# Kernel tuning notes

Measured on AMD Instinct MI355X. Metric: run time of the kernel, lower is better.

The kernel has to match this reference:

```python
import jax, jax.numpy as jnp
import numpy as np

EPS = 1e-5

def layernorm(x, w, b):
    mu = jnp.mean(x, axis=-1, keepdims=True)
    xc = x - mu
    var = jnp.mean(xc * xc, axis=-1, keepdims=True)
    return xc * jax.lax.rsqrt(var + EPS) * w + b

def setup_inputs() -> dict:
    key = jax.random.key(0)
    ks = jax.random.split(key, 9)
    B, T, Nm, Nl = 8, 8, 1024, 64
    Vw, Tw, H, Dh = 1024, 2048, 8, 64
    inner = H * Dh  # 512
    s_q = 1.0 / np.sqrt(Tw)
    s_kv = 1.0 / np.sqrt(Vw)
    s_o = 1.0 / np.sqrt(inner)
    return {
        "x": jax.random.normal(ks[0], (B, T, Nm, Vw), jnp.float32),
        "latents": jax.random.normal(ks[1], (B, T, Nl, Tw), jnp.float32),
        "nm_w": jnp.ones((Vw,), jnp.float32),
        "nm_b": jnp.zeros((Vw,), jnp.float32),
        "nl_w": jnp.ones((Tw,), jnp.float32),
        "nl_b": jnp.zeros((Tw,), jnp.float32),
        "Wq": jax.random.normal(ks[2], (Tw, inner), jnp.float32) * s_q,
        "Wkv": jax.random.normal(ks[3], (Vw, 2 * inner), jnp.float32) * s_kv,
        "Wout": jax.random.normal(ks[4], (inner, Tw), jnp.float32) * s_o,
    }

def reference(x, latents, nm_w, nm_b, nl_w, nl_b, Wq, Wkv, Wout):
    H, Dh = 8, 64
    scale = Dh ** (-0.5)
    B, T, Nm, _ = x.shape
    Nl = latents.shape[2]
    xn = layernorm(x, nm_w, nm_b)          # (B,T,Nm,Vw)
    ln = layernorm(latents, nl_w, nl_b)    # (B,T,Nl,Tw)
    q = (ln @ Wq).reshape(B, T, Nl, H, Dh)           # b t i h d
    kv = xn @ Wkv                                     # (B,T,Nm,2*inner)
    k, v = jnp.split(kv, 2, axis=-1)
    k = k.reshape(B, T, Nm, H, Dh)                    # b t j h d
    v = v.reshape(B, T, Nm, H, Dh)
    sim = jnp.einsum('btihd,btjhd->bthij', q * scale, k)  # (B,T,H,Nl,Nm)
    attn = jax.nn.softmax(sim, axis=-1)
    out = jnp.einsum('bthij,btjhd->btihd', attn, v)       # (B,T,Nl,H,Dh)
    out = out.reshape(B, T, Nl, H * Dh)
    return out @ Wout                                     # (B,T,Nl,Tw)
```

## Files before the change

### kernel.cpp

```cpp
#include <hip/hip_runtime.h>

typedef __attribute__((ext_vector_type(8))) short bfrag8;
typedef __attribute__((ext_vector_type(4))) float f32x4;

typedef const unsigned int __attribute__((address_space(1)))* gas1_u32;
typedef unsigned int __attribute__((address_space(3)))* gas3_u32;

#define DEV __device__ __forceinline__

DEV unsigned short f2bf(float f) {
  unsigned int u = __builtin_bit_cast(unsigned int, f);
  u += 0x7fffu + ((u >> 16) & 1u);
  return (unsigned short)(u >> 16);
}

DEV void gload_lds16(const void* g, void* l) {
  __builtin_amdgcn_global_load_lds((gas1_u32)g, (gas3_u32)l, 16, 0, 0);
}

template<int N> DEV void gate_bar();
template<> DEV void gate_bar<4>() { asm volatile("s_waitcnt vmcnt(4)\n\ts_barrier" ::: "memory"); }
template<> DEV void gate_bar<6>() { asm volatile("s_waitcnt vmcnt(6)\n\ts_barrier" ::: "memory"); }
template<> DEV void gate_bar<8>() { asm volatile("s_waitcnt vmcnt(8)\n\ts_barrier" ::: "memory"); }

__global__ __launch_bounds__(256) void k_xstats(
    const float* __restrict__ x, unsigned short* __restrict__ xb,
    float* __restrict__ mu, float* __restrict__ rstd)
{
  const int wid = threadIdx.x >> 6, lane = threadIdx.x & 63;
  const int row = blockIdx.x * 4 + wid;
  const float* base = x + (size_t)row * 1024;
  float4 v[4];
  #pragma unroll
  for (int i = 0; i < 4; ++i) v[i] = ((const float4*)base)[i * 64 + lane];
  float s = 0.f, q = 0.f;
  #pragma unroll
  for (int i = 0; i < 4; ++i) {
    s += v[i].x + v[i].y + v[i].z + v[i].w;
    q += v[i].x*v[i].x + v[i].y*v[i].y + v[i].z*v[i].z + v[i].w*v[i].w;
  }
  #pragma unroll
  for (int off = 32; off >= 1; off >>= 1) { s += __shfl_xor(s, off); q += __shfl_xor(q, off); }
  const float m  = s * (1.0f/1024.0f);
  const float var = q * (1.0f/1024.0f) - m * m;
  const float rs = rsqrtf(var + 1e-5f);
  if (lane == 0) { mu[row] = m; rstd[row] = rs; }
  unsigned short* ob = xb + (size_t)row * 1024;
  #pragma unroll
  for (int i = 0; i < 4; ++i) {
    ushort4 o;
    o.x = f2bf(v[i].x); o.y = f2bf(v[i].y); o.z = f2bf(v[i].z); o.w = f2bf(v[i].w);
    ((ushort4*)ob)[i * 64 + lane] = o;
  }
}

__global__ __launch_bounds__(256) void k_lnlat(
    const float* __restrict__ lat, const float* __restrict__ w,
    const float* __restrict__ b, unsigned short* __restrict__ ln)
{
  const int row = blockIdx.x, tid = threadIdx.x;
  const float* base = lat + (size_t)row * 2048;
  const float4 v0 = ((const float4*)base)[tid];
  const float4 v1 = ((const float4*)base)[256 + tid];
  float s = v0.x+v0.y+v0.z+v0.w + v1.x+v1.y+v1.z+v1.w;
  float q = v0.x*v0.x+v0.y*v0.y+v0.z*v0.z+v0.w*v0.w
          + v1.x*v1.x+v1.y*v1.y+v1.z*v1.z+v1.w*v1.w;
  #pragma unroll
  for (int off = 32; off >= 1; off >>= 1) { s += __shfl_xor(s, off); q += __shfl_xor(q, off); }
  __shared__ float red[8];
  const int wid = tid >> 6, lane = tid & 63;
  if (lane == 0) { red[wid] = s; red[4 + wid] = q; }
  __syncthreads();
  s = red[0] + red[1] + red[2] + red[3];
  q = red[4] + red[5] + red[6] + red[7];
  const float m  = s * (1.0f/2048.0f);
  const float var = q * (1.0f/2048.0f) - m * m;
  const float rs = rsqrtf(var + 1e-5f);
  const float4 w0 = ((const float4*)w)[tid], w1 = ((const float4*)w)[256 + tid];
  const float4 b0 = ((const float4*)b)[tid], b1 = ((const float4*)b)[256 + tid];
  ushort4 o0, o1;
  o0.x = f2bf((v0.x - m) * rs * w0.x + b0.x);
  o0.y = f2bf((v0.y - m) * rs * w0.y + b0.y);
  o0.z = f2bf((v0.z - m) * rs * w0.z + b0.z);
  o0.w = f2bf((v0.w - m) * rs * w0.w + b0.w);
  o1.x = f2bf((v1.x - m) * rs * w1.x + b1.x);
  o1.y = f2bf((v1.y - m) * rs * w1.y + b1.y);
  o1.z = f2bf((v1.z - m) * rs * w1.z + b1.z);
  o1.w = f2bf((v1.w - m) * rs * w1.w + b1.w);
  ((ushort4*)(ln + (size_t)row * 2048))[tid] = o0;
  ((ushort4*)(ln + (size_t)row * 2048))[256 + tid] = o1;
}

__global__ __launch_bounds__(256) void k_transpose_cast(
    const float* __restrict__ src, unsigned short* __restrict__ dst,
    int K, int N, const float* __restrict__ rowscale, float scale)
{
  __shared__ float tile[32][33];
  const int tx = threadIdx.x & 31, ty = threadIdx.x >> 5;
  const int ntiles = N >> 5;
  const int k0 = (blockIdx.x / ntiles) << 5;
  const int n0 = (blockIdx.x % ntiles) << 5;
  #pragma unroll
  for (int r = 0; r < 4; ++r) {
    const int kk = ty + r * 8;
    float v = src[(size_t)(k0 + kk) * N + n0 + tx] * scale;
    if (rowscale) v *= rowscale[k0 + kk];
    tile[kk][tx] = v;
  }
  __syncthreads();
  #pragma unroll
  for (int r = 0; r < 4; ++r) {
    const int nn = ty + r * 8;
    dst[(size_t)(n0 + nn) * K + k0 + tx] = f2bf(tile[tx][nn]);
  }
}

__global__ __launch_bounds__(256) void k_c1c2_part(
    const float* __restrict__ Wkv, const float* __restrict__ w,
    const float* __restrict__ b, float* __restrict__ part)
{
  const int kc = blockIdx.x;
  const int n  = blockIdx.y * 256 + threadIdx.x;
  float s1 = 0.f, s2 = 0.f;
  const int k0 = kc * 64;
  for (int k = k0; k < k0 + 64; ++k) {
    const float wv = Wkv[(size_t)k * 1024 + n];
    s1 += w[k] * wv;
    s2 += b[k] * wv;
  }
  part[(size_t)(kc * 2 + 0) * 1024 + n] = s1;
  part[(size_t)(kc * 2 + 1) * 1024 + n] = s2;
}

__global__ __launch_bounds__(256) void k_c1c2_red(
    const float* __restrict__ part, float* __restrict__ c1, float* __restrict__ c2)
{
  const int n = blockIdx.x * 256 + threadIdx.x;
  float s1 = 0.f, s2 = 0.f;
  #pragma unroll
  for (int kc = 0; kc < 16; ++kc) {
    s1 += part[(size_t)(kc * 2 + 0) * 1024 + n];
    s2 += part[(size_t)(kc * 2 + 1) * 1024 + n];
  }
  c1[n] = s1; c2[n] = s2;
}

#define BAR8   __builtin_amdgcn_s_barrier()
#define GATE4  gate_bar<4>()

__global__ __launch_bounds__(512, 2) void k_gemm8(
    const unsigned short* __restrict__ A,
    const unsigned short* __restrict__ Bt,
    unsigned short* __restrict__ C,
    const float* __restrict__ mu, const float* __restrict__ rstd,
    const float* __restrict__ c1, const float* __restrict__ c2)
{
  constexpr int NKT = 16;
  __shared__ __attribute__((aligned(16))) char lds[131072];

  int bid = blockIdx.x;
  { const int nwg = gridDim.x; const int q = nwg >> 3; bid = (bid & 7) * q + (bid >> 3); }
  const int mt = bid >> 2, nt = bid & 3;
  const int tid = threadIdx.x;
  const int wid = tid >> 6, lane = tid & 63;
  const int g = lane >> 4, c = lane & 15;
  const int wr = wid >> 2, wc = wid & 3;
  const int MO = wr * 128, NO = wc * 64;

  const unsigned short* gA = A + (size_t)mt * 256 * 1024;
  const unsigned short* gB = Bt + (size_t)nt * 256 * 1024;

  const f32x4 zz = {0.f, 0.f, 0.f, 0.f};
  f32x4 acc[8][4];
  #pragma unroll
  for (int m = 0; m < 8; ++m)
    #pragma unroll
    for (int n = 0; n < 4; ++n) acc[m][n] = zz;

  auto stageA = [&](int buf, int kk, int kt) {
    #pragma unroll
    for (int i = 0; i < 2; ++i) {
      const int o = (i * 512 + tid) * 16;
      const int row = o >> 6;
      const int ss = ((((o >> 4) & 3) - (row >> 1)) & 3);
      gload_lds16((const char*)(gA + (size_t)row * 1024 + kt * 64 + kk * 32) + ss * 16,
                  lds + buf * 32768 + kk * 16384 + o);
    }
  };
  auto stageB = [&](int buf, int kk, int kt) {
    #pragma unroll
    for (int i = 0; i < 2; ++i) {
      const int o = (i * 512 + tid) * 16;
      const int row = o >> 6;
      const int ss = ((((o >> 4) & 3) - (row >> 1)) & 3);
      gload_lds16((const char*)(gB + (size_t)row * 1024 + kt * 64 + kk * 32) + ss * 16,
                  lds + 65536 + buf * 32768 + kk * 16384 + o);
    }
  };
  auto rdA = [&](int buf, int kk, int m) -> bfrag8 {
    const int row = MO + m * 16 + c;
    return *(const bfrag8*)(lds + buf * 32768 + kk * 16384 + row * 64
                            + (((g + (row >> 1)) & 3) << 4));
  };
  auto rdB = [&](int buf, int kk, int n) -> bfrag8 {
    const int row = NO + n * 16 + c;
    return *(const bfrag8*)(lds + 65536 + buf * 32768 + kk * 16384 + row * 64
                            + (((g + (row >> 1)) & 3) << 4));
  };

  bfrag8 a[8], b0[4], b1[4];

  auto tile4 = [&](int buf, int sb, int ukt) {
    #pragma unroll
    for (int m = 0; m < 8; ++m) a[m] = rdA(buf, 0, m);
    #pragma unroll
    for (int n = 0; n < 4; ++n) b0[n] = rdB(buf, 0, n);
    stageA(sb, 0, ukt);
    __builtin_amdgcn_s_setprio(1);
    #pragma unroll
    for (int m = 0; m < 8; ++m) {
      acc[m][0] = __builtin_amdgcn_mfma_f32_16x16x32_bf16(a[m], b0[0], acc[m][0], 0, 0, 0);
      acc[m][1] = __builtin_amdgcn_mfma_f32_16x16x32_bf16(a[m], b0[1], acc[m][1], 0, 0, 0);
    }
    __builtin_amdgcn_s_setprio(0);
    GATE4;
    #pragma unroll
    for (int n = 0; n < 4; ++n) b1[n] = rdB(buf, 1, n);
    stageB(sb, 0, ukt);
    __builtin_amdgcn_s_setprio(1);
    #pragma unroll
    for (int m = 0; m < 8; ++m) {
      acc[m][2] = __builtin_amdgcn_mfma_f32_16x16x32_bf16(a[m], b0[2], acc[m][2], 0, 0, 0);
      acc[m][3] = __builtin_amdgcn_mfma_f32_16x16x32_bf16(a[m], b0[3], acc[m][3], 0, 0, 0);
    }
    __builtin_amdgcn_s_setprio(0);
    GATE4;
    #pragma unroll
    for (int m = 0; m < 8; ++m) a[m] = rdA(buf, 1, m);
    stageB(sb, 1, ukt);
    __builtin_amdgcn_s_setprio(1);
    #pragma unroll
    for (int m = 0; m < 8; ++m) {
      acc[m][0] = __builtin_amdgcn_mfma_f32_16x16x32_bf16(a[m], b1[0], acc[m][0], 0, 0, 0);
      acc[m][1] = __builtin_amdgcn_mfma_f32_16x16x32_bf16(a[m], b1[1], acc[m][1], 0, 0, 0);
    }
    __builtin_amdgcn_s_setprio(0);
    BAR8;
    stageA(sb, 1, ukt);
    __builtin_amdgcn_s_setprio(1);
    #pragma unroll
    for (int m = 0; m < 8; ++m) {
      acc[m][2] = __builtin_amdgcn_mfma_f32_16x16x32_bf16(a[m], b1[2], acc[m][2], 0, 0, 0);
      acc[m][3] = __builtin_amdgcn_mfma_f32_16x16x32_bf16(a[m], b1[3], acc[m][3], 0, 0, 0);
    }
    __builtin_amdgcn_s_setprio(0);
    GATE4;
  };

  stageA(0, 0, 0); stageB(0, 0, 0); stageB(0, 1, 0); stageA(0, 1, 0);
  GATE4;

  for (int t = 0; t < NKT; t += 2) {
    const int u2 = (t + 2 < NKT) ? t + 2 : 0;
    tile4(0, 1, t + 1);
    tile4(1, 0, u2);
  }
  asm volatile("s_waitcnt vmcnt(0)" ::: "memory");

  #pragma unroll
  for (int m = 0; m < 8; ++m) {
    #pragma unroll
    for (int j = 0; j < 4; ++j) {
      const size_t orow = (size_t)mt * 256 + MO + m * 16 + g * 4 + j;
      const float rs = rstd[orow], muv = mu[orow];
      #pragma unroll
      for (int n = 0; n < 4; ++n) {
        const int gcol = nt * 256 + NO + n * 16 + c;
        const float v = rs * (acc[m][n][j] - muv * c1[gcol]) + c2[gcol];
        C[orow * 1024 + gcol] = f2bf(v);
      }
    }
  }
}

template<int BM, int BN, int WM, int WN, int NT, int MODE>
__global__ __launch_bounds__(NT, 2) void k_gemm(
    const unsigned short* __restrict__ A, int lda,
    const unsigned short* __restrict__ Bt, int ldb,
    int K, int mtiles, int ntiles,
    void* __restrict__ Cout, int ldc)
{
  constexpr int BK = 32;
  constexpr int NW = NT / 64;
  constexpr int MF = (BM / WM) / 16;
  constexpr int NF = (BN / WN) / 16;
  constexpr int LA = (BM * BK) / (8 * NT);
  constexpr int LB = (BN * BK) / (8 * NT);
  constexpr int LPS = LA + LB;
  constexpr int RA = BM * BK;
  constexpr int RB = BN * BK;
  static_assert(WM * WN == NW, "wave grid");
  static_assert(LA >= 1 && LB >= 1, "tile too small for NT");
  static_assert(LPS == 3 || LPS == 4, "gate specialization");

  __shared__ __attribute__((aligned(16))) unsigned short As[4 * RA];
  __shared__ __attribute__((aligned(16))) unsigned short Bs[4 * RB];

  int bid = blockIdx.x;
  {
    const int nwg = gridDim.x;
    if ((nwg & 7) == 0) {
      const int q = nwg >> 3;
      bid = (bid & 7) * q + (bid >> 3);
    }
  }
  const int mt = bid / ntiles, nt = bid % ntiles;
  const int tid = threadIdx.x;
  const int wid = tid >> 6, lane = tid & 63;
  const int g = lane >> 4, c = lane & 15;
  const int wr = wid / WN, wc = wid % WN;
  const int MO = wr * (BM / WM), NO = wc * (BN / WN);
  const int rot = (c >> 1) & 3;

  const unsigned short* gA = A + (size_t)mt * BM * lda;
  const unsigned short* gB = Bt + (size_t)nt * BN * ldb;

  const f32x4 zz = {0.f, 0.f, 0.f, 0.f};
  f32x4 acc[MF][NF];
  #pragma unroll
  for (int m = 0; m < MF; ++m)
    #pragma unroll
    for (int n = 0; n < NF; ++n) acc[m][n] = zz;

  auto stage = [&](int R, int kt) {
    #pragma unroll
    for (int i = 0; i < LA; ++i) {
      const int o = (i * NT + tid) * 16;
      const int row = o >> 6;
      const int slot = (o >> 4) & 3;
      const int srcb = (((slot - ((row >> 1) & 3)) & 3) << 4);
      gload_lds16((const char*)(gA + (size_t)row * lda + kt * BK) + srcb,
                  (char*)(As + R * RA) + o);
    }
    #pragma unroll
    for (int i = 0; i < LB; ++i) {
      const int o = (i * NT + tid) * 16;
      const int row = o >> 6;
      const int slot = (o >> 4) & 3;
      const int srcb = (((slot - ((row >> 1) & 3)) & 3) << 4);
      gload_lds16((const char*)(gB + (size_t)row * ldb + kt * BK) + srcb,
                  (char*)(Bs + R * RB) + o);
    }
  };

  auto compute = [&](int R) {
    const char* as = (const char*)(As + R * RA);
    const char* bs = (const char*)(Bs + R * RB);
    bfrag8 af[MF], bf[NF];
    #pragma unroll
    for (int m = 0; m < MF; ++m) {
      const int rw = MO + m * 16 + c;
      af[m] = *(const bfrag8*)(as + rw * 64 + (((g + rot) & 3) << 4));
    }
    #pragma unroll
    for (int n = 0; n < NF; ++n) {
      const int rw = NO + n * 16 + c;
      bf[n] = *(const bfrag8*)(bs + rw * 64 + (((g + rot) & 3) << 4));
    }
    #pragma unroll
    for (int m = 0; m < MF; ++m)
      #pragma unroll
      for (int n = 0; n < NF; ++n)
        acc[m][n] = __builtin_amdgcn_mfma_f32_16x16x32_bf16(af[m], bf[n], acc[m][n], 0, 0, 0);
  };

  const int nkt = K / BK;
  stage(0, 0); stage(1, 1); stage(2, 2);
  for (int t = 0; t < nkt; t += 4) {
    #pragma unroll
    for (int r = 0; r < 4; ++r) {
      int t3 = t + r + 3; if (t3 >= nkt) t3 -= nkt;
      gate_bar<2 * LPS>();
      stage((r + 3) & 3, t3);
      compute(r);
    }
  }
  asm volatile("s_waitcnt vmcnt(0)" ::: "memory");

  #pragma unroll
  for (int m = 0; m < MF; ++m) {
    #pragma unroll
    for (int j = 0; j < 4; ++j) {
      const size_t orow = (size_t)mt * BM + MO + m * 16 + g * 4 + j;
      #pragma unroll
      for (int n = 0; n < NF; ++n) {
        const int gcol = nt * BN + NO + n * 16 + c;
        const float v = acc[m][n][j];
        if constexpr (MODE == 2) ((float*)Cout)[orow * ldc + gcol] = v;
        else ((unsigned short*)Cout)[orow * ldc + gcol] = f2bf(v);
      }
    }
  }
}

__global__ __launch_bounds__(256) void k_attn(
    const unsigned short* __restrict__ q,
    const unsigned short* __restrict__ kv,
    unsigned short* __restrict__ ao)
{
  __shared__ __attribute__((aligned(16))) unsigned short Vt[64 * 64];
  const int bid = blockIdx.x;
  const int bt = bid >> 3, h = bid & 7;
  const int tid = threadIdx.x;
  const int wid = tid >> 6, lane = tid & 63;
  const int g = lane >> 4, c = lane & 15;

  const size_t qoff = ((size_t)bt * 64 + wid * 16 + c) * 512 + h * 64;
  const bfrag8 qf0 = *(const bfrag8*)(q + qoff + g * 8);
  const bfrag8 qf1 = *(const bfrag8*)(q + qoff + 32 + g * 8);

  const f32x4 zz = {0.f, 0.f, 0.f, 0.f};
  f32x4 o[4] = {zz, zz, zz, zz};
  float m_run = -1e30f, l_run = 0.f;

  const size_t kvbase = (size_t)bt * 1024 * 1024;
  const unsigned short* kbase = kv + kvbase + h * 64;
  const unsigned short* vbase = kv + kvbase + 512 + h * 64;

  for (int ch = 0; ch < 16; ++ch) {
    #pragma unroll
    for (int rr = 0; rr < 2; ++rr) {
      const int key = rr * 32 + (tid >> 3);
      const int d0 = (tid & 7) * 8;
      const bfrag8 vv = *(const bfrag8*)(vbase + (size_t)(ch * 64 + key) * 1024 + d0);
      #pragma unroll
      for (int j = 0; j < 8; ++j)
        Vt[(d0 + j) * 64 + (key ^ (j << 3))] = (unsigned short)vv[j];
    }
    __syncthreads();
    #pragma unroll
    for (int ks = 0; ks < 2; ++ks) {
      const int kb = ch * 64 + ks * 32;
      f32x4 s[2];
      #pragma unroll
      for (int t = 0; t < 2; ++t) {
        const int kr = ((c >> 2) << 3) + (t << 2) + (c & 3);
        const unsigned short* krow = kbase + (size_t)(kb + kr) * 1024;
        s[t] = zz;
        s[t] = __builtin_amdgcn_mfma_f32_16x16x32_bf16(*(const bfrag8*)(krow + g * 8),      qf0, s[t], 0, 0, 0);
        s[t] = __builtin_amdgcn_mfma_f32_16x16x32_bf16(*(const bfrag8*)(krow + 32 + g * 8), qf1, s[t], 0, 0, 0);
      }
      float pm = s[0][0];
      #pragma unroll
      for (int i = 1; i < 4; ++i) pm = fmaxf(pm, s[0][i]);
      #pragma unroll
      for (int i = 0; i < 4; ++i) pm = fmaxf(pm, s[1][i]);
      pm = fmaxf(pm, __shfl_xor(pm, 16));
      pm = fmaxf(pm, __shfl_xor(pm, 32));
      const float mn = fmaxf(m_run, pm);
      const float alpha = __expf(m_run - mn);
      float p[8];
      #pragma unroll
      for (int i = 0; i < 4; ++i) p[i]     = __expf(s[0][i] - mn);
      #pragma unroll
      for (int i = 0; i < 4; ++i) p[4 + i] = __expf(s[1][i] - mn);
      float ts = 0.f;
      #pragma unroll
      for (int i = 0; i < 8; ++i) ts += p[i];
      ts += __shfl_xor(ts, 16);
      ts += __shfl_xor(ts, 32);
      l_run = l_run * alpha + ts;
      m_run = mn;
      float ar[4];
      #pragma unroll
      for (int rj = 0; rj < 4; ++rj) ar[rj] = __shfl(alpha, g * 4 + rj);
      #pragma unroll
      for (int db = 0; db < 4; ++db)
        #pragma unroll
        for (int j = 0; j < 4; ++j) o[db][j] *= ar[j];
      bfrag8 pa;
      #pragma unroll
      for (int i = 0; i < 8; ++i) pa[i] = (short)f2bf(p[i]);
      #pragma unroll
      for (int db = 0; db < 4; ++db) {
        const int d = db * 16 + c;
        const bfrag8 vb = *(const bfrag8*)(Vt + d * 64 + ((ks * 32 + g * 8) ^ ((c & 7) << 3)));
        o[db] = __builtin_amdgcn_mfma_f32_16x16x32_bf16(pa, vb, o[db], 0, 0, 0);
      }
    }
    __syncthreads();
  }
  float lr[4];
  #pragma unroll
  for (int rj = 0; rj < 4; ++rj) lr[rj] = __shfl(l_run, g * 4 + rj);
  #pragma unroll
  for (int db = 0; db < 4; ++db)
    #pragma unroll
    for (int j = 0; j < 4; ++j) {
      const float val = o[db][j] / lr[j];
      ao[((size_t)bt * 64 + wid * 16 + g * 4 + j) * 512 + h * 64 + db * 16 + c] = f2bf(val);
    }
}

extern "C" void kernel_launch(void* const* d_in, const int* in_sizes, int n_in,
                              void* d_out, int out_size, void* d_ws, size_t ws_size,
                              hipStream_t stream)
{
  const float* x    = (const float*)d_in[0];
  const float* lat  = (const float*)d_in[1];
  const float* nm_w = (const float*)d_in[2];
  const float* nm_b = (const float*)d_in[3];
  const float* nl_w = (const float*)d_in[4];
  const float* nl_b = (const float*)d_in[5];
  const float* Wq   = (const float*)d_in[6];
  const float* Wkv  = (const float*)d_in[7];
  const float* Wout = (const float*)d_in[8];

  char* p = (char*)d_ws;
  auto take = [&](size_t bytes) { char* r = p; p += (bytes + 255) & ~(size_t)255; return r; };
  unsigned short* xb    = (unsigned short*)take(64ull * 1024 * 1024 * 2);
  unsigned short* kvb   = (unsigned short*)take(64ull * 1024 * 1024 * 2);
  unsigned short* lnb   = (unsigned short*)take(4096ull * 2048 * 2);
  unsigned short* qbuf  = (unsigned short*)take(4096ull * 512 * 2);
  unsigned short* aob   = (unsigned short*)take(4096ull * 512 * 2);
  unsigned short* WqT   = (unsigned short*)take(512ull * 2048 * 2);
  unsigned short* WkvT  = (unsigned short*)take(1024ull * 1024 * 2);
  unsigned short* WoutT = (unsigned short*)take(2048ull * 512 * 2);
  float* muv  = (float*)take(65536ull * 4);
  float* rsd  = (float*)take(65536ull * 4);
  float* c1   = (float*)take(1024 * 4);
  float* c2   = (float*)take(1024 * 4);
  float* part = (float*)take(32ull * 1024 * 4);
  if ((size_t)(p - (char*)d_ws) > ws_size) return;

  k_transpose_cast<<<dim3(64 * 16), 256, 0, stream>>>(Wq,   WqT,   2048,  512, nullptr, 0.125f);
  k_transpose_cast<<<dim3(32 * 32), 256, 0, stream>>>(Wkv,  WkvT,  1024, 1024, nm_w,    1.0f);
  k_transpose_cast<<<dim3(16 * 64), 256, 0, stream>>>(Wout, WoutT,  512, 2048, nullptr, 1.0f);
  k_c1c2_part<<<dim3(16, 4), 256, 0, stream>>>(Wkv, nm_w, nm_b, part);
  k_c1c2_red<<<dim3(4), 256, 0, stream>>>(part, c1, c2);
  k_xstats<<<dim3(16384), 256, 0, stream>>>(x, xb, muv, rsd);
  k_lnlat<<<dim3(4096), 256, 0, stream>>>(lat, nl_w, nl_b, lnb);

  k_gemm8<<<dim3(1024), 512, 0, stream>>>(xb, WkvT, kvb, muv, rsd, c1, c2);
  k_gemm<64, 128, 1, 4, 256, 1><<<dim3(256), 256, 0, stream>>>(
      lnb, 2048, WqT, 2048, 2048, 64, 4, qbuf, 512);

  k_attn<<<dim3(512), 256, 0, stream>>>(qbuf, kvb, aob);

  k_gemm<64, 128, 1, 4, 256, 2><<<dim3(1024), 256, 0, stream>>>(
      aob, 512, WoutT, 512, 512, 64, 16, d_out, 2048);
}
```

Baseline: 378.3 us.

## Write K/V/Q in head-major layout and fold latent layernorm into Q GEMM epilogue

The KV and Q GEMM epilogues now write outputs in a head-major (bt,h,j,d) layout, so attention reads K and V rows with a 64-element stride instead of 1024, giving contiguous per-head tiles. The latent layernorm is replaced by the shared stats kernel (raw bf16 cast plus mu/rstd), with nl_w folded into WqT and the mean/bias corrections applied through c1q/c2q in the Q GEMM epilogue. This removes the separate normalize pass and improves attention locality, at the cost of scattered epilogue stores and bf16 rounding of un-normalized latents.

```diff
diff --git a/kernel.cpp b/kernel.cpp
--- a/kernel.cpp
+++ b/kernel.cpp
@@ -23,72 +23,37 @@
 template<> DEV void gate_bar<6>() { asm volatile("s_waitcnt vmcnt(6)\n\ts_barrier" ::: "memory"); }
 template<> DEV void gate_bar<8>() { asm volatile("s_waitcnt vmcnt(8)\n\ts_barrier" ::: "memory"); }
 
-__global__ __launch_bounds__(256) void k_xstats(
+template<int W>
+__global__ __launch_bounds__(256) void k_stats(
     const float* __restrict__ x, unsigned short* __restrict__ xb,
     float* __restrict__ mu, float* __restrict__ rstd)
 {
+  constexpr int NV = W / 256;
   const int wid = threadIdx.x >> 6, lane = threadIdx.x & 63;
   const int row = blockIdx.x * 4 + wid;
-  const float* base = x + (size_t)row * 1024;
-  float4 v[4];
-  #pragma unroll
-  for (int i = 0; i < 4; ++i) v[i] = ((const float4*)base)[i * 64 + lane];
+  const float* base = x + (size_t)row * W;
+  float4 v[NV];
+  #pragma unroll
+  for (int i = 0; i < NV; ++i) v[i] = ((const float4*)base)[i * 64 + lane];
   float s = 0.f, q = 0.f;
   #pragma unroll
-  for (int i = 0; i < 4; ++i) {
+  for (int i = 0; i < NV; ++i) {
     s += v[i].x + v[i].y + v[i].z + v[i].w;
     q += v[i].x*v[i].x + v[i].y*v[i].y + v[i].z*v[i].z + v[i].w*v[i].w;
   }
   #pragma unroll
   for (int off = 32; off >= 1; off >>= 1) { s += __shfl_xor(s, off); q += __shfl_xor(q, off); }
-  const float m  = s * (1.0f/1024.0f);
-  const float var = q * (1.0f/1024.0f) - m * m;
-  const float rs = rsqrtf(var + 1e-5f);
+  const float m   = s * (1.0f / W);
+  const float var = q * (1.0f / W) - m * m;
+  const float rs  = rsqrtf(var + 1e-5f);
   if (lane == 0) { mu[row] = m; rstd[row] = rs; }
-  unsigned short* ob = xb + (size_t)row * 1024;
-  #pragma unroll
-  for (int i = 0; i < 4; ++i) {
+  unsigned short* ob = xb + (size_t)row * W;
+  #pragma unroll
+  for (int i = 0; i < NV; ++i) {
     ushort4 o;
     o.x = f2bf(v[i].x); o.y = f2bf(v[i].y); o.z = f2bf(v[i].z); o.w = f2bf(v[i].w);
     ((ushort4*)ob)[i * 64 + lane] = o;
   }
-}
-
-__global__ __launch_bounds__(256) void k_lnlat(
-    const float* __restrict__ lat, const float* __restrict__ w,
-    const float* __restrict__ b, unsigned short* __restrict__ ln)
-{
-  const int row = blockIdx.x, tid = threadIdx.x;
-  const float* base = lat + (size_t)row * 2048;
-  const float4 v0 = ((const float4*)base)[tid];
-  const float4 v1 = ((const float4*)base)[256 + tid];
-  float s = v0.x+v0.y+v0.z+v0.w + v1.x+v1.y+v1.z+v1.w;
-  float q = v0.x*v0.x+v0.y*v0.y+v0.z*v0.z+v0.w*v0.w
-          + v1.x*v1.x+v1.y*v1.y+v1.z*v1.z+v1.w*v1.w;
-  #pragma unroll
-  for (int off = 32; off >= 1; off >>= 1) { s += __shfl_xor(s, off); q += __shfl_xor(q, off); }
-  __shared__ float red[8];
-  const int wid = tid >> 6, lane = tid & 63;
-  if (lane == 0) { red[wid] = s; red[4 + wid] = q; }
-  __syncthreads();
-  s = red[0] + red[1] + red[2] + red[3];
-  q = red[4] + red[5] + red[6] + red[7];
-  const float m  = s * (1.0f/2048.0f);
-  const float var = q * (1.0f/2048.0f) - m * m;
-  const float rs = rsqrtf(var + 1e-5f);
-  const float4 w0 = ((const float4*)w)[tid], w1 = ((const float4*)w)[256 + tid];
-  const float4 b0 = ((const float4*)b)[tid], b1 = ((const float4*)b)[256 + tid];
-  ushort4 o0, o1;
-  o0.x = f2bf((v0.x - m) * rs * w0.x + b0.x);
-  o0.y = f2bf((v0.y - m) * rs * w0.y + b0.y);
-  o0.z = f2bf((v0.z - m) * rs * w0.z + b0.z);
-  o0.w = f2bf((v0.w - m) * rs * w0.w + b0.w);
-  o1.x = f2bf((v1.x - m) * rs * w1.x + b1.x);
-  o1.y = f2bf((v1.y - m) * rs * w1.y + b1.y);
-  o1.z = f2bf((v1.z - m) * rs * w1.z + b1.z);
-  o1.w = f2bf((v1.w - m) * rs * w1.w + b1.w);
-  ((ushort4*)(ln + (size_t)row * 2048))[tid] = o0;
-  ((ushort4*)(ln + (size_t)row * 2048))[256 + tid] = o1;
 }
 
 __global__ __launch_bounds__(256) void k_transpose_cast(
@@ -116,31 +81,31 @@
 }
 
 __global__ __launch_bounds__(256) void k_c1c2_part(
-    const float* __restrict__ Wkv, const float* __restrict__ w,
-    const float* __restrict__ b, float* __restrict__ part)
+    const float* __restrict__ Wm, const float* __restrict__ w,
+    const float* __restrict__ b, float* __restrict__ part, int N, float scale)
 {
   const int kc = blockIdx.x;
   const int n  = blockIdx.y * 256 + threadIdx.x;
   float s1 = 0.f, s2 = 0.f;
   const int k0 = kc * 64;
   for (int k = k0; k < k0 + 64; ++k) {
-    const float wv = Wkv[(size_t)k * 1024 + n];
+    const float wv = Wm[(size_t)k * N + n];
     s1 += w[k] * wv;
     s2 += b[k] * wv;
   }
-  part[(size_t)(kc * 2 + 0) * 1024 + n] = s1;
-  part[(size_t)(kc * 2 + 1) * 1024 + n] = s2;
+  part[(size_t)(kc * 2 + 0) * N + n] = s1 * scale;
+  part[(size_t)(kc * 2 + 1) * N + n] = s2 * scale;
 }
 
 __global__ __launch_bounds__(256) void k_c1c2_red(
-    const float* __restrict__ part, float* __restrict__ c1, float* __restrict__ c2)
+    const float* __restrict__ part, float* __restrict__ c1, float* __restrict__ c2,
+    int nchunks, int N)
 {
   const int n = blockIdx.x * 256 + threadIdx.x;
   float s1 = 0.f, s2 = 0.f;
-  #pragma unroll
-  for (int kc = 0; kc < 16; ++kc) {
-    s1 += part[(size_t)(kc * 2 + 0) * 1024 + n];
-    s2 += part[(size_t)(kc * 2 + 1) * 1024 + n];
+  for (int kc = 0; kc < nchunks; ++kc) {
+    s1 += part[(size_t)(kc * 2 + 0) * N + n];
+    s2 += part[(size_t)(kc * 2 + 1) * N + n];
   }
   c1[n] = s1; c2[n] = s2;
 }
@@ -151,7 +116,7 @@
 __global__ __launch_bounds__(512, 2) void k_gemm8(
     const unsigned short* __restrict__ A,
     const unsigned short* __restrict__ Bt,
-    unsigned short* __restrict__ C,
+    unsigned short* __restrict__ Chm,
     const float* __restrict__ mu, const float* __restrict__ rstd,
     const float* __restrict__ c1, const float* __restrict__ c2)
 {
@@ -272,12 +237,14 @@
     #pragma unroll
     for (int j = 0; j < 4; ++j) {
       const size_t orow = (size_t)mt * 256 + MO + m * 16 + g * 4 + j;
+      const int btn = (int)(orow >> 10), jj = (int)(orow & 1023);
+      const size_t pbase = ((size_t)(btn * 16 + nt * 4 + wc)) * 65536 + (size_t)jj * 64;
       const float rs = rstd[orow], muv = mu[orow];
       #pragma unroll
       for (int n = 0; n < 4; ++n) {
         const int gcol = nt * 256 + NO + n * 16 + c;
         const float v = rs * (acc[m][n][j] - muv * c1[gcol]) + c2[gcol];
-        C[orow * 1024 + gcol] = f2bf(v);
+        Chm[pbase + n * 16 + c] = f2bf(v);
       }
     }
   }
@@ -288,7 +255,9 @@
     const unsigned short* __restrict__ A, int lda,
     const unsigned short* __restrict__ Bt, int ldb,
     int K, int mtiles, int ntiles,
-    void* __restrict__ Cout, int ldc)
+    void* __restrict__ Cout, int ldc,
+    const float* __restrict__ mu, const float* __restrict__ rstd,
+    const float* __restrict__ c1, const float* __restrict__ c2)
 {
   constexpr int BK = 32;
   constexpr int NW = NT / 64;
@@ -392,20 +361,28 @@
     #pragma unroll
     for (int j = 0; j < 4; ++j) {
       const size_t orow = (size_t)mt * BM + MO + m * 16 + g * 4 + j;
+      float rs = 0.f, muv = 0.f;
+      if constexpr (MODE == 1) { rs = rstd[orow]; muv = mu[orow]; }
       #pragma unroll
       for (int n = 0; n < NF; ++n) {
         const int gcol = nt * BN + NO + n * 16 + c;
-        const float v = acc[m][n][j];
-        if constexpr (MODE == 2) ((float*)Cout)[orow * ldc + gcol] = v;
-        else ((unsigned short*)Cout)[orow * ldc + gcol] = f2bf(v);
+        float v = acc[m][n][j];
+        if constexpr (MODE == 1) {
+          v = rs * (v - muv * c1[gcol]) + c2[gcol];
+          const int bt = (int)(orow >> 6), ii = (int)(orow & 63);
+          const int h = gcol >> 6, d = gcol & 63;
+          ((unsigned short*)Cout)[(size_t)(bt * 8 + h) * 4096 + ii * 64 + d] = f2bf(v);
+        } else {
+          ((float*)Cout)[orow * ldc + gcol] = v;
+        }
       }
     }
   }
 }
 
 __global__ __launch_bounds__(256) void k_attn(
-    const unsigned short* __restrict__ q,
-    const unsigned short* __restrict__ kv,
+    const unsigned short* __restrict__ q2,
+    const unsigned short* __restrict__ kv2,
     unsigned short* __restrict__ ao)
 {
   __shared__ __attribute__((aligned(16))) unsigned short Vt[64 * 64];
@@ -415,24 +392,23 @@
   const int wid = tid >> 6, lane = tid & 63;
   const int g = lane >> 4, c = lane & 15;
 
-  const size_t qoff = ((size_t)bt * 64 + wid * 16 + c) * 512 + h * 64;
-  const bfrag8 qf0 = *(const bfrag8*)(q + qoff + g * 8);
-  const bfrag8 qf1 = *(const bfrag8*)(q + qoff + 32 + g * 8);
+  const size_t qoff = ((size_t)(bt * 8 + h) * 64 + wid * 16 + c) * 64;
+  const bfrag8 qf0 = *(const bfrag8*)(q2 + qoff + g * 8);
+  const bfrag8 qf1 = *(const bfrag8*)(q2 + qoff + 32 + g * 8);
 
   const f32x4 zz = {0.f, 0.f, 0.f, 0.f};
   f32x4 o[4] = {zz, zz, zz, zz};
   float m_run = -1e30f, l_run = 0.f;
 
-  const size_t kvbase = (size_t)bt * 1024 * 1024;
-  const unsigned short* kbase = kv + kvbase + h * 64;
-  const unsigned short* vbase = kv + kvbase + 512 + h * 64;
+  const unsigned short* kbase = kv2 + (size_t)(bt * 16 + h) * 65536;
+  const unsigned short* vbase = kv2 + (size_t)(bt * 16 + 8 + h) * 65536;
 
   for (int ch = 0; ch < 16; ++ch) {
     #pragma unroll
     for (int rr = 0; rr < 2; ++rr) {
       const int key = rr * 32 + (tid >> 3);
       const int d0 = (tid & 7) * 8;
-      const bfrag8 vv = *(const bfrag8*)(vbase + (size_t)(ch * 64 + key) * 1024 + d0);
+      const bfrag8 vv = *(const bfrag8*)(vbase + (size_t)(ch * 64 + key) * 64 + d0);
       #pragma unroll
       for (int j = 0; j < 8; ++j)
         Vt[(d0 + j) * 64 + (key ^ (j << 3))] = (unsigned short)vv[j];
@@ -445,7 +421,7 @@
       #pragma unroll
       for (int t = 0; t < 2; ++t) {
         const int kr = ((c >> 2) << 3) + (t << 2) + (c & 3);
-        const unsigned short* krow = kbase + (size_t)(kb + kr) * 1024;
+        const unsigned short* krow = kbase + (size_t)(kb + kr) * 64;
         s[t] = zz;
         s[t] = __builtin_amdgcn_mfma_f32_16x16x32_bf16(*(const bfrag8*)(krow + g * 8),      qf0, s[t], 0, 0, 0);
         s[t] = __builtin_amdgcn_mfma_f32_16x16x32_bf16(*(const bfrag8*)(krow + 32 + g * 8), qf1, s[t], 0, 0, 0);
@@ -520,7 +496,7 @@
   auto take = [&](size_t bytes) { char* r = p; p += (bytes + 255) & ~(size_t)255; return r; };
   unsigned short* xb    = (unsigned short*)take(64ull * 1024 * 1024 * 2);
   unsigned short* kvb   = (unsigned short*)take(64ull * 1024 * 1024 * 2);
-  unsigned short* lnb   = (unsigned short*)take(4096ull * 2048 * 2);
+  unsigned short* latb  = (unsigned short*)take(4096ull * 2048 * 2);
   unsigned short* qbuf  = (unsigned short*)take(4096ull * 512 * 2);
   unsigned short* aob   = (unsigned short*)take(4096ull * 512 * 2);
   unsigned short* WqT   = (unsigned short*)take(512ull * 2048 * 2);
@@ -528,25 +504,33 @@
   unsigned short* WoutT = (unsigned short*)take(2048ull * 512 * 2);
   float* muv  = (float*)take(65536ull * 4);
   float* rsd  = (float*)take(65536ull * 4);
+  float* mul  = (float*)take(4096ull * 4);
+  float* rsl  = (float*)take(4096ull * 4);
   float* c1   = (float*)take(1024 * 4);
   float* c2   = (float*)take(1024 * 4);
-  float* part = (float*)take(32ull * 1024 * 4);
+  float* c1q  = (float*)take(512 * 4);
+  float* c2q  = (float*)take(512 * 4);
+  float* part  = (float*)take(32ull * 1024 * 4);
+  float* part2 = (float*)take(64ull * 512 * 4);
   if ((size_t)(p - (char*)d_ws) > ws_size) return;
 
-  k_transpose_cast<<<dim3(64 * 16), 256, 0, stream>>>(Wq,   WqT,   2048,  512, nullptr, 0.125f);
-  k_transpose_cast<<<dim3(32 * 32), 256, 0, stream>>>(Wkv,  WkvT,  1024, 1024, nm_w,    1.0f);
+  k_transpose_cast<<<dim3(64 * 16), 256, 0, stream>>>(Wq,   WqT,   2048,  512, nl_w, 0.125f);
+  k_transpose_cast<<<dim3(32 * 32), 256, 0, stream>>>(Wkv,  WkvT,  1024, 1024, nm_w, 1.0f);
   k_transpose_cast<<<dim3(16 * 64), 256, 0, stream>>>(Wout, WoutT,  512, 2048, nullptr, 1.0f);
-  k_c1c2_part<<<dim3(16, 4), 256, 0, stream>>>(Wkv, nm_w, nm_b, part);
-  k_c1c2_red<<<dim3(4), 256, 0, stream>>>(part, c1, c2);
-  k_xstats<<<dim3(16384), 256, 0, stream>>>(x, xb, muv, rsd);
-  k_lnlat<<<dim3(4096), 256, 0, stream>>>(lat, nl_w, nl_b, lnb);
+  k_c1c2_part<<<dim3(16, 4), 256, 0, stream>>>(Wkv, nm_w, nm_b, part, 1024, 1.0f);
+  k_c1c2_red<<<dim3(4), 256, 0, stream>>>(part, c1, c2, 16, 1024);
+  k_c1c2_part<<<dim3(32, 2), 256, 0, stream>>>(Wq, nl_w, nl_b, part2, 512, 0.125f);
+  k_c1c2_red<<<dim3(2), 256, 0, stream>>>(part2, c1q, c2q, 32, 512);
+  k_stats<1024><<<dim3(16384), 256, 0, stream>>>(x, xb, muv, rsd);
+  k_stats<2048><<<dim3(1024), 256, 0, stream>>>(lat, latb, mul, rsl);
 
   k_gemm8<<<dim3(1024), 512, 0, stream>>>(xb, WkvT, kvb, muv, rsd, c1, c2);
   k_gemm<64, 128, 1, 4, 256, 1><<<dim3(256), 256, 0, stream>>>(
-      lnb, 2048, WqT, 2048, 2048, 64, 4, qbuf, 512);
+      latb, 2048, WqT, 2048, 2048, 64, 4, qbuf, 512, mul, rsl, c1q, c2q);
 
   k_attn<<<dim3(512), 256, 0, stream>>>(qbuf, kvb, aob);
 
   k_gemm<64, 128, 1, 4, 256, 2><<<dim3(1024), 256, 0, stream>>>(
-      aob, 512, WoutT, 512, 512, 64, 16, d_out, 2048);
-}
+      aob, 512, WoutT, 512, 512, 64, 16, d_out, 2048,
+      nullptr, nullptr, nullptr, nullptr);
+}
```

Measured after the change: 398.4 us. 1.05x slower.

## Fuse x layernorm statistics and bf16 cast into the KV GEMM A-loader

Applied to the files above, without the earlier changes.

Removes the separate k_xstats pass that read the fp32 x, wrote a bf16 copy plus per-row mean and rstd, which the KV GEMM then reread. The GEMM now loads fp32 x directly into registers, converts to bf16 and writes swizzled LDS tiles itself, accumulating row sum and sum of squares along the way, and reduces the stats into shared memory for the epilogue. This cuts a full bf16 write and read of the 64M-element activation. In exchange the A operand moves through registers instead of direct-to-LDS loads, which raises register pressure and VALU work inside the MFMA loop. The pipeline also changes from two k-tiles per loop iteration to one, with new wait and barrier points. Each GEMM block reads its 256-row fp32 slice of x once per N tile (4 N tiles), so x traffic is fp32 rather than bf16.

```diff
diff --git a/kernel.cpp b/kernel.cpp
--- a/kernel.cpp
+++ b/kernel.cpp
@@ -19,40 +19,8 @@
 }
 
 template<int N> DEV void gate_bar();
-template<> DEV void gate_bar<4>() { asm volatile("s_waitcnt vmcnt(4)\n\ts_barrier" ::: "memory"); }
 template<> DEV void gate_bar<6>() { asm volatile("s_waitcnt vmcnt(6)\n\ts_barrier" ::: "memory"); }
 template<> DEV void gate_bar<8>() { asm volatile("s_waitcnt vmcnt(8)\n\ts_barrier" ::: "memory"); }
-
-__global__ __launch_bounds__(256) void k_xstats(
-    const float* __restrict__ x, unsigned short* __restrict__ xb,
-    float* __restrict__ mu, float* __restrict__ rstd)
-{
-  const int wid = threadIdx.x >> 6, lane = threadIdx.x & 63;
-  const int row = blockIdx.x * 4 + wid;
-  const float* base = x + (size_t)row * 1024;
-  float4 v[4];
-  #pragma unroll
-  for (int i = 0; i < 4; ++i) v[i] = ((const float4*)base)[i * 64 + lane];
-  float s = 0.f, q = 0.f;
-  #pragma unroll
-  for (int i = 0; i < 4; ++i) {
-    s += v[i].x + v[i].y + v[i].z + v[i].w;
-    q += v[i].x*v[i].x + v[i].y*v[i].y + v[i].z*v[i].z + v[i].w*v[i].w;
-  }
-  #pragma unroll
-  for (int off = 32; off >= 1; off >>= 1) { s += __shfl_xor(s, off); q += __shfl_xor(q, off); }
-  const float m  = s * (1.0f/1024.0f);
-  const float var = q * (1.0f/1024.0f) - m * m;
-  const float rs = rsqrtf(var + 1e-5f);
-  if (lane == 0) { mu[row] = m; rstd[row] = rs; }
-  unsigned short* ob = xb + (size_t)row * 1024;
-  #pragma unroll
-  for (int i = 0; i < 4; ++i) {
-    ushort4 o;
-    o.x = f2bf(v[i].x); o.y = f2bf(v[i].y); o.z = f2bf(v[i].z); o.w = f2bf(v[i].w);
-    ((ushort4*)ob)[i * 64 + lane] = o;
-  }
-}
 
 __global__ __launch_bounds__(256) void k_lnlat(
     const float* __restrict__ lat, const float* __restrict__ w,
@@ -145,18 +113,15 @@
   c1[n] = s1; c2[n] = s2;
 }
 
-#define BAR8   __builtin_amdgcn_s_barrier()
-#define GATE4  gate_bar<4>()
-
-__global__ __launch_bounds__(512, 2) void k_gemm8(
-    const unsigned short* __restrict__ A,
+__global__ __launch_bounds__(512, 2) void k_gemm8f(
+    const float* __restrict__ X,
     const unsigned short* __restrict__ Bt,
     unsigned short* __restrict__ C,
-    const float* __restrict__ mu, const float* __restrict__ rstd,
     const float* __restrict__ c1, const float* __restrict__ c2)
 {
   constexpr int NKT = 16;
   __shared__ __attribute__((aligned(16))) char lds[131072];
+  __shared__ float sstat[256][2];
 
   int bid = blockIdx.x;
   { const int nwg = gridDim.x; const int q = nwg >> 3; bid = (bid & 7) * q + (bid >> 3); }
@@ -167,8 +132,12 @@
   const int wr = wid >> 2, wc = wid & 3;
   const int MO = wr * 128, NO = wc * 64;
 
-  const unsigned short* gA = A + (size_t)mt * 256 * 1024;
   const unsigned short* gB = Bt + (size_t)nt * 256 * 1024;
+  const int arow = tid >> 1, asl = tid & 1;
+  const int rho = (arow >> 1) & 3;
+  const int ps0 = (2 * asl + 0 + rho) & 3;
+  const int ps1 = (2 * asl + 1 + rho) & 3;
+  const float* gX = X + (size_t)(mt * 256 + arow) * 1024 + asl * 16;
 
   const f32x4 zz = {0.f, 0.f, 0.f, 0.f};
   f32x4 acc[8][4];
@@ -177,15 +146,31 @@
     #pragma unroll
     for (int n = 0; n < 4; ++n) acc[m][n] = zz;
 
-  auto stageA = [&](int buf, int kk, int kt) {
-    #pragma unroll
-    for (int i = 0; i < 2; ++i) {
-      const int o = (i * 512 + tid) * 16;
-      const int row = o >> 6;
-      const int ss = ((((o >> 4) & 3) - (row >> 1)) & 3);
-      gload_lds16((const char*)(gA + (size_t)row * 1024 + kt * 64 + kk * 32) + ss * 16,
-                  lds + buf * 32768 + kk * 16384 + o);
-    }
+  float4 ax[2][4];
+  float ssum = 0.f, sq = 0.f;
+
+  auto loadA = [&](int kt) {
+    #pragma unroll
+    for (int kk = 0; kk < 2; ++kk)
+      #pragma unroll
+      for (int i = 0; i < 4; ++i)
+        ax[kk][i] = *(const float4*)(gX + (size_t)kt * 64 + kk * 32 + i * 4);
+  };
+  auto putA = [&](int buf, int kk, int accum) {
+    unsigned int w[8];
+    #pragma unroll
+    for (int i = 0; i < 4; ++i) {
+      const float4 v = ax[kk][i];
+      if (accum) {
+        ssum += v.x + v.y + v.z + v.w;
+        sq   += v.x*v.x + v.y*v.y + v.z*v.z + v.w*v.w;
+      }
+      w[2*i]   = (unsigned)f2bf(v.x) | ((unsigned)f2bf(v.y) << 16);
+      w[2*i+1] = (unsigned)f2bf(v.z) | ((unsigned)f2bf(v.w) << 16);
+    }
+    char* base = lds + buf * 32768 + kk * 16384 + arow * 64;
+    *(uint4*)(base + ps0 * 16) = make_uint4(w[0], w[1], w[2], w[3]);
+    *(uint4*)(base + ps1 * 16) = make_uint4(w[4], w[5], w[6], w[7]);
   };
   auto stageB = [&](int buf, int kk, int kt) {
     #pragma unroll
@@ -210,12 +195,13 @@
 
   bfrag8 a[8], b0[4], b1[4];
 
-  auto tile4 = [&](int buf, int sb, int ukt) {
+  auto tile4 = [&](int buf, int sb, int ukt, int accum) {
     #pragma unroll
     for (int m = 0; m < 8; ++m) a[m] = rdA(buf, 0, m);
     #pragma unroll
     for (int n = 0; n < 4; ++n) b0[n] = rdB(buf, 0, n);
-    stageA(sb, 0, ukt);
+    loadA(ukt);
+    stageB(sb, 0, ukt);
     __builtin_amdgcn_s_setprio(1);
     #pragma unroll
     for (int m = 0; m < 8; ++m) {
@@ -223,10 +209,11 @@
       acc[m][1] = __builtin_amdgcn_mfma_f32_16x16x32_bf16(a[m], b0[1], acc[m][1], 0, 0, 0);
     }
     __builtin_amdgcn_s_setprio(0);
-    GATE4;
+    asm volatile("s_waitcnt vmcnt(10)\n\ts_barrier" ::: "memory");
     #pragma unroll
     for (int n = 0; n < 4; ++n) b1[n] = rdB(buf, 1, n);
-    stageB(sb, 0, ukt);
+    putA(sb, 0, accum);
+    stageB(sb, 1, ukt);
     __builtin_amdgcn_s_setprio(1);
     #pragma unroll
     for (int m = 0; m < 8; ++m) {
@@ -234,10 +221,10 @@
       acc[m][3] = __builtin_amdgcn_mfma_f32_16x16x32_bf16(a[m], b0[3], acc[m][3], 0, 0, 0);
     }
     __builtin_amdgcn_s_setprio(0);
-    GATE4;
+    asm volatile("s_barrier" ::: "memory");
     #pragma unroll
     for (int m = 0; m < 8; ++m) a[m] = rdA(buf, 1, m);
-    stageB(sb, 1, ukt);
+    putA(sb, 1, accum);
     __builtin_amdgcn_s_setprio(1);
     #pragma unroll
     for (int m = 0; m < 8; ++m) {
@@ -245,8 +232,7 @@
       acc[m][1] = __builtin_amdgcn_mfma_f32_16x16x32_bf16(a[m], b1[1], acc[m][1], 0, 0, 0);
     }
     __builtin_amdgcn_s_setprio(0);
-    BAR8;
-    stageA(sb, 1, ukt);
+    asm volatile("s_barrier" ::: "memory");
     __builtin_amdgcn_s_setprio(1);
     #pragma unroll
     for (int m = 0; m < 8; ++m) {
@@ -254,25 +240,37 @@
       acc[m][3] = __builtin_amdgcn_mfma_f32_16x16x32_bf16(a[m], b1[3], acc[m][3], 0, 0, 0);
     }
     __builtin_amdgcn_s_setprio(0);
-    GATE4;
-  };
-
-  stageA(0, 0, 0); stageB(0, 0, 0); stageB(0, 1, 0); stageA(0, 1, 0);
-  GATE4;
-
-  for (int t = 0; t < NKT; t += 2) {
-    const int u2 = (t + 2 < NKT) ? t + 2 : 0;
-    tile4(0, 1, t + 1);
-    tile4(1, 0, u2);
-  }
-  asm volatile("s_waitcnt vmcnt(0)" ::: "memory");
+    asm volatile("s_waitcnt vmcnt(2) lgkmcnt(0)\n\ts_barrier" ::: "memory");
+  };
+
+  loadA(0);
+  putA(0, 0, 1); putA(0, 1, 1);
+  stageB(0, 0, 0); stageB(0, 1, 0);
+  asm volatile("s_waitcnt vmcnt(0) lgkmcnt(0)\n\ts_barrier" ::: "memory");
+
+  for (int t = 0; t < NKT; ++t) {
+    const int real = (t + 1 < NKT);
+    tile4(t & 1, (t & 1) ^ 1, real ? t + 1 : 0, real);
+  }
+  asm volatile("s_waitcnt vmcnt(0) lgkmcnt(0)" ::: "memory");
+
+  ssum += __shfl_xor(ssum, 1);
+  sq   += __shfl_xor(sq, 1);
+  if (asl == 0) {
+    const float m = ssum * (1.0f / 1024.0f);
+    const float var = sq * (1.0f / 1024.0f) - m * m;
+    sstat[arow][0] = m;
+    sstat[arow][1] = rsqrtf(var + 1e-5f);
+  }
+  __syncthreads();
 
   #pragma unroll
   for (int m = 0; m < 8; ++m) {
     #pragma unroll
     for (int j = 0; j < 4; ++j) {
-      const size_t orow = (size_t)mt * 256 + MO + m * 16 + g * 4 + j;
-      const float rs = rstd[orow], muv = mu[orow];
+      const int rl = MO + m * 16 + g * 4 + j;
+      const size_t orow = (size_t)mt * 256 + rl;
+      const float muv = sstat[rl][0], rs = sstat[rl][1];
       #pragma unroll
       for (int n = 0; n < 4; ++n) {
         const int gcol = nt * 256 + NO + n * 16 + c;
@@ -518,7 +516,6 @@
 
   char* p = (char*)d_ws;
   auto take = [&](size_t bytes) { char* r = p; p += (bytes + 255) & ~(size_t)255; return r; };
-  unsigned short* xb    = (unsigned short*)take(64ull * 1024 * 1024 * 2);
   unsigned short* kvb   = (unsigned short*)take(64ull * 1024 * 1024 * 2);
   unsigned short* lnb   = (unsigned short*)take(4096ull * 2048 * 2);
   unsigned short* qbuf  = (unsigned short*)take(4096ull * 512 * 2);
@@ -526,8 +523,6 @@
   unsigned short* WqT   = (unsigned short*)take(512ull * 2048 * 2);
   unsigned short* WkvT  = (unsigned short*)take(1024ull * 1024 * 2);
   unsigned short* WoutT = (unsigned short*)take(2048ull * 512 * 2);
-  float* muv  = (float*)take(65536ull * 4);
-  float* rsd  = (float*)take(65536ull * 4);
   float* c1   = (float*)take(1024 * 4);
   float* c2   = (float*)take(1024 * 4);
   float* part = (float*)take(32ull * 1024 * 4);
@@ -538,10 +533,9 @@
   k_transpose_cast<<<dim3(16 * 64), 256, 0, stream>>>(Wout, WoutT,  512, 2048, nullptr, 1.0f);
   k_c1c2_part<<<dim3(16, 4), 256, 0, stream>>>(Wkv, nm_w, nm_b, part);
   k_c1c2_red<<<dim3(4), 256, 0, stream>>>(part, c1, c2);
-  k_xstats<<<dim3(16384), 256, 0, stream>>>(x, xb, muv, rsd);
   k_lnlat<<<dim3(4096), 256, 0, stream>>>(lat, nl_w, nl_b, lnb);
 
-  k_gemm8<<<dim3(1024), 512, 0, stream>>>(xb, WkvT, kvb, muv, rsd, c1, c2);
+  k_gemm8f<<<dim3(1024), 512, 0, stream>>>(x, WkvT, kvb, c1, c2);
   k_gemm<64, 128, 1, 4, 256, 1><<<dim3(256), 256, 0, stream>>>(
       lnb, 2048, WqT, 2048, 2048, 64, 4, qbuf, 512);
 
```

After: 897.1 us. +137.2%, slower.
